# Optimization experiments

Measured on AMD Instinct MI355X. Metric: run time of the kernel, lower is better.

The kernel has to match this reference:

```python
import jax, jax.numpy as jnp
import numpy as np

D_MODEL = 2048
MLP = 8192
E = 8
R = 16
ALPHA = 32
SCALING = ALPHA / R  # lora_alpha / rank


def setup_inputs() -> dict:
    key = jax.random.key(0)
    ks = jax.random.split(key, 16)
    s = 0.02
    return {
        "x": jax.random.normal(ks[0], (4, 1024, D_MODEL), dtype=jnp.float32),
        # frozen base weights (nn.Linear stores [out, in])
        "w_gate": jax.random.normal(ks[1], (MLP, D_MODEL), dtype=jnp.float32) * s,
        "w_up": jax.random.normal(ks[2], (MLP, D_MODEL), dtype=jnp.float32) * s,
        "w_down": jax.random.normal(ks[3], (D_MODEL, MLP), dtype=jnp.float32) * s,
        # router
        "router_w": jax.random.normal(ks[4], (E, D_MODEL), dtype=jnp.float32) * s,
        "router_b": jnp.zeros((E,), dtype=jnp.float32),
        # LoRA expert params: A [E, r, fan_in], B [E, fan_out, r]
        "A_gate": jax.random.normal(ks[5], (E, R, D_MODEL), dtype=jnp.float32) * s,
        "B_gate": jax.random.normal(ks[6], (E, MLP, R), dtype=jnp.float32) * s,
        "A_up": jax.random.normal(ks[7], (E, R, D_MODEL), dtype=jnp.float32) * s,
        "B_up": jax.random.normal(ks[8], (E, MLP, R), dtype=jnp.float32) * s,
        "A_down": jax.random.normal(ks[9], (E, R, MLP), dtype=jnp.float32) * s,
        "B_down": jax.random.normal(ks[10], (E, D_MODEL, R), dtype=jnp.float32) * s,
    }


def _lora_moe_sparse(inp, W, A, B, onehot):
    # inp: [B,S,din], W: [dout,din], A: [E,r,din], B: [E,dout,r], onehot: [B,S,E]
    base = jnp.einsum("bsd,od->bso", inp, W)
    # low-rank projection for every expert is tiny: [B,S,E,r]
    t = jnp.einsum("bsd,erd->bser", inp, A)
    # top-1 dispatch: onehot zeroes out non-selected experts (== scatter assign,
    # since each token has exactly one expert)
    lora = jnp.einsum("bser,bse,eor->bso", t, onehot, B) * SCALING
    return base + lora


def reference(x, w_gate, w_up, w_down, router_w, router_b,
              A_gate, B_gate, A_up, B_up, A_down, B_down):
    logits = jnp.einsum("bsd,ed->bse", x, router_w) + router_b
    routing = jax.nn.softmax(logits, axis=-1)
    index = jnp.argmax(routing, axis=-1)                 # [B,S]
    y_hard = jax.nn.one_hot(index, E, dtype=logits.dtype)  # [B,S,E]
    expert_choice = y_hard - jax.lax.stop_gradient(routing) + routing

    gate_out = _lora_moe_sparse(x, w_gate, A_gate, B_gate, y_hard)
    up_out = _lora_moe_sparse(x, w_up, A_up, B_up, y_hard)
    h = jax.nn.silu(gate_out) * up_out
    out = _lora_moe_sparse(h, w_down, A_down, B_down, y_hard)
    return (out, routing, expert_choice)
```

## Files before the change

kernel.cpp:

```cpp
#include <hip/hip_runtime.h>
#include <stdint.h>

#define NTOK   4096
#define DM     2048
#define DMLP   8192
#define NEXP   8
#define NRANK  16
#define SCAL   2.0f

#define LDXA 2304
#define LDHA 8320

typedef __bf16 bf16x8 __attribute__((ext_vector_type(8)));
typedef float  f32x4  __attribute__((ext_vector_type(4)));
typedef unsigned short u16;

__device__ __forceinline__ u16 f2bf(float f) {
  unsigned u = __float_as_uint(f);
  u += 0x7fffu + ((u >> 16) & 1u);
  return (u16)(u >> 16);
}

__device__ __forceinline__ void gload_lds16(const void* g, void* l) {
  __builtin_amdgcn_global_load_lds((const __attribute__((address_space(1))) void*)g,
                                   (__attribute__((address_space(3))) void*)l, 16, 0, 0);
}

__global__ void cvt_kernel(const float* __restrict__ src, u16* __restrict__ dst, int n4) {
  int i = blockIdx.x * blockDim.x + threadIdx.x;
  int stride = gridDim.x * blockDim.x;
  for (; i < n4; i += stride) {
    float4 v = ((const float4*)src)[i];
    ushort4 o;
    o.x = f2bf(v.x); o.y = f2bf(v.y); o.z = f2bf(v.z); o.w = f2bf(v.w);
    ((ushort4*)dst)[i] = o;
  }
}

__global__ void build_wx(const float* __restrict__ W,
                         const float* __restrict__ Bm,
                         u16* __restrict__ dst,
                         int din, int ldx, int extoff, int browstride) {
  const int o = blockIdx.x;
  const int tid = threadIdx.x;
  u16* drow = dst + (size_t)o * ldx;
  const float* wrow = W + (size_t)o * din;
  for (int c4 = tid; c4 < din / 4; c4 += 256) {
    float4 v = ((const float4*)wrow)[c4];
    ushort4 ov;
    ov.x = f2bf(v.x); ov.y = f2bf(v.y); ov.z = f2bf(v.z); ov.w = f2bf(v.w);
    ((ushort4*)drow)[c4] = ov;
  }
  const int next = ldx - din;
  if (tid < next) {
    int c = tid;
    u16 val = 0;
    if (c >= extoff && c < extoff + NEXP * NRANK) {
      int ce = c - extoff;
      int e = ce >> 4, r = ce & 15;
      val = f2bf(Bm[((size_t)e * browstride + o) * NRANK + r]);
    }
    drow[din + c] = val;
  }
}

__global__ void router_kernel(const float* __restrict__ x,
                              const float* __restrict__ rw,
                              const float* __restrict__ rb,
                              u16* __restrict__ xa,
                              int* __restrict__ idx,
                              float* __restrict__ out_rout,
                              float* __restrict__ out_ec) {
  const int wave = threadIdx.x >> 6;
  const int lane = threadIdx.x & 63;
  const int m = blockIdx.x * 4 + wave;

  const float4* xrow = (const float4*)(x + (size_t)m * DM + lane * 32);
  float4 xv[8];
#pragma unroll
  for (int i = 0; i < 8; ++i) xv[i] = xrow[i];

  uint4 o[4];
  unsigned* op = (unsigned*)o;
#pragma unroll
  for (int i = 0; i < 8; ++i) {
    op[2*i]   = (unsigned)f2bf(xv[i].x) | ((unsigned)f2bf(xv[i].y) << 16);
    op[2*i+1] = (unsigned)f2bf(xv[i].z) | ((unsigned)f2bf(xv[i].w) << 16);
  }
  uint4* xdst = (uint4*)(xa + (size_t)m * LDXA + lane * 32);
#pragma unroll
  for (int i = 0; i < 4; ++i) xdst[i] = o[i];

  float lg[NEXP];
#pragma unroll
  for (int e = 0; e < NEXP; ++e) {
    const float4* wrow = (const float4*)(rw + (size_t)e * DM + lane * 32);
    float s = 0.f;
#pragma unroll
    for (int i = 0; i < 8; ++i) {
      float4 wv = wrow[i];
      s += xv[i].x*wv.x + xv[i].y*wv.y + xv[i].z*wv.z + xv[i].w*wv.w;
    }
#pragma unroll
    for (int off = 32; off > 0; off >>= 1) s += __shfl_xor(s, off, 64);
    lg[e] = s + rb[e];
  }

  float mx = lg[0];
#pragma unroll
  for (int e = 1; e < NEXP; ++e) mx = fmaxf(mx, lg[e]);
  float ex[NEXP], se = 0.f;
#pragma unroll
  for (int e = 0; e < NEXP; ++e) { ex[e] = expf(lg[e] - mx); se += ex[e]; }
  float inv = 1.f / se;
  int best = 0; float bv = lg[0];
#pragma unroll
  for (int e = 1; e < NEXP; ++e) if (lg[e] > bv) { bv = lg[e]; best = e; }

  if (lane == 0) {
    idx[m] = best;
#pragma unroll
    for (int e = 0; e < NEXP; ++e) {
      float r = ex[e] * inv;
      out_rout[(size_t)m * NEXP + e] = r;
      float hard = (e == best) ? 1.f : 0.f;
      out_ec[(size_t)m * NEXP + e] = (hard - r) + r;
    }
  }
}

template<int MODE>
__global__ __launch_bounds__(256, 2)
void gemm_kernel(const u16* __restrict__ A,
                 const u16* __restrict__ B0,
                 const int* __restrict__ idx,
                 void* __restrict__ Cout)
{
  constexpr int LDA = (MODE == 0) ? LDXA : LDHA;
  constexpr int LDB = (MODE == 0) ? 2048 : 8192;
  constexpr int NKI = (MODE == 0) ? 64 : 32;

  __shared__ u16 lds[16384];

  const int tid = threadIdx.x;
  const int w = tid >> 6;
  const int l = tid & 63;
  const int wm = w >> 1, wn = w & 1;
  const int mtile = blockIdx.x;
  const int ntile = (MODE == 3) ? 0 : (int)blockIdx.y;
  const int ks    = (MODE == 3) ? (int)blockIdx.y : 0;
  const int kb0   = (MODE == 3) ? ks * 1024 : 0;

  int srow[2];
  srow[0] = w * 16 + (l >> 2);
  srow[1] = 64 + srow[0];
  const int chunk = (l & 3) ^ ((srow[0] >> 1) & 3);
  const int scol = chunk * 8;

  const u16* aptr[2];
  const u16* bptr[2];
#pragma unroll
  for (int i = 0; i < 2; ++i) {
    aptr[i] = A + (size_t)(mtile * 128 + srow[i]) * LDA + kb0 + scol;
    bptr[i] = B0 + (size_t)(ntile * 128 + srow[i]) * LDB + kb0 + scol;
  }

  char* ldsc = (char*)lds;
  auto stage = [&](int buf, int kt) {
    const int kk = kt * 32;
    char* base = ldsc + buf * 16384;
#pragma unroll
    for (int i = 0; i < 2; ++i) {
      gload_lds16(aptr[i] + kk, base + i * 4096 + w * 1024);
      gload_lds16(bptr[i] + kk, base + 8192 + i * 4096 + w * 1024);
    }
  };

  f32x4 acc[4][4];
  f32x4 zf = {0.f, 0.f, 0.f, 0.f};
#pragma unroll
  for (int a = 0; a < 4; ++a)
#pragma unroll
    for (int b = 0; b < 4; ++b) acc[a][b] = zf;

  stage(0, 0);
  __syncthreads();

  const int kq   = l >> 4;
  const int arow = wm * 64 + (l & 15);
  const int brow = wn * 64 + (l & 15);
  const int axor = (kq ^ ((arow >> 1) & 3)) << 4;
  const int bxor = (kq ^ ((brow >> 1) & 3)) << 4;

  for (int kt = 0; kt < NKI; ++kt) {
    const int buf = kt & 1;
    if (kt + 1 < NKI) stage(buf ^ 1, kt + 1);
    const char* bA = ldsc + buf * 16384;
    const char* bB = bA + 8192;
    bf16x8 af[4], bfr[4];
#pragma unroll
    for (int fm = 0; fm < 4; ++fm)
      af[fm] = *(const bf16x8*)(bA + (arow + fm * 16) * 64 + axor);
#pragma unroll
    for (int fn = 0; fn < 4; ++fn)
      bfr[fn] = *(const bf16x8*)(bB + (brow + fn * 16) * 64 + bxor);
#pragma unroll
    for (int fm = 0; fm < 4; ++fm)
#pragma unroll
      for (int fn = 0; fn < 4; ++fn)
        acc[fm][fn] = __builtin_amdgcn_mfma_f32_16x16x32_bf16(af[fm], bfr[fn], acc[fm][fn], 0, 0, 0);
    __syncthreads();
  }

  const int lq = l >> 4;
  const int lr = l & 15;

  if (MODE == 0) {
    u16* X = (u16*)Cout;
#pragma unroll
    for (int fm = 0; fm < 4; ++fm)
#pragma unroll
      for (int fn = 0; fn < 4; ++fn)
        for (int j = 0; j < 4; ++j) {
          int m = mtile * 128 + wm * 64 + fm * 16 + lq * 4 + j;
          int c = ntile * 128 + wn * 64 + fn * 16 + lr;
          int e = idx[m];
          u16 v = (((c & 127) >> 4) == e) ? f2bf(SCAL * acc[fm][fn][j]) : (u16)0;
          X[(size_t)m * LDXA + 2048 + c] = v;
        }
  } else {
    float* P = (float*)Cout + (size_t)ks * NTOK * 128;
#pragma unroll
    for (int fm = 0; fm < 4; ++fm)
#pragma unroll
      for (int fn = 0; fn < 4; ++fn)
        for (int j = 0; j < 4; ++j) {
          int m = mtile * 128 + wm * 64 + fm * 16 + lq * 4 + j;
          int c = wn * 64 + fn * 16 + lr;
          P[(size_t)m * 128 + c] = acc[fm][fn][j];
        }
  }
}

__global__ __launch_bounds__(512, 2)
void gemm_gu(const u16* __restrict__ Ag,
             const u16* __restrict__ B0g,
             const u16* __restrict__ B1g,
             u16* __restrict__ H)
{
  constexpr int NKT = 36;
  __shared__ char L[131072];

  const int tid = threadIdx.x, w = tid >> 6, l = tid & 63;
  const int wm = w >> 2, wn = w & 3;
  const int bid = blockIdx.x;
  const int rr = bid >> 3;
  const int mtile = rr >> 3;
  const int ntile = (bid & 7) * 8 + (rr & 7);

  const u16 *agb0, *agb1, *bgb0, *bgb1;
  {
    int row0 = tid >> 2, row1 = 128 + row0;
    int lc = (tid & 3) ^ ((row0 >> 1) & 3);
    agb0 = Ag + (size_t)(mtile * 256 + row0) * LDXA + lc * 8;
    agb1 = Ag + (size_t)(mtile * 256 + row1) * LDXA + lc * 8;
    int c0 = ntile * 128 + ((row0 >> 5) << 4) + (row0 & 15);
    int c1 = ntile * 128 + ((row1 >> 5) << 4) + (row1 & 15);
    bgb0 = (((row0 >> 4) & 1) ? B1g : B0g) + (size_t)c0 * LDXA + lc * 8;
    bgb1 = (((row1 >> 4) & 1) ? B1g : B0g) + (size_t)c1 * LDXA + lc * 8;
  }
  const int sdst = w * 1024;

#define STGA(z, kt) { const int ko_ = ((kt) < NKT ? (kt) : NKT - 1) * 64 + ((z) & 1) * 32; \
    gload_lds16(agb0 + ko_, L + (z) * 16384 + sdst); \
    gload_lds16(agb1 + ko_, L + (z) * 16384 + 8192 + sdst); }
#define STGB(z, kt) { const int ko_ = ((kt) < NKT ? (kt) : NKT - 1) * 64 + ((z) & 1) * 32; \
    gload_lds16(bgb0 + ko_, L + 65536 + (z) * 16384 + sdst); \
    gload_lds16(bgb1 + ko_, L + 65536 + (z) * 16384 + 8192 + sdst); }

  const int lr = l & 15;
  const int kob = (((l >> 4) ^ ((lr >> 1) & 3)) << 4);
  const int abase = (wm * 128 + lr) * 64 + kob;
  const int bbase = (wn * 64 + lr) * 64 + kob;

  bf16x8 A0_[4], A1_[4], B0_[4], B1_[4];
#define RDA(S, z, qa) _Pragma("unroll") for (int f = 0; f < 4; ++f) \
    S[f] = *(const bf16x8*)(L + (z) * 16384 + abase + (qa) * 4096 + f * 1024);
#define RDB(S, z) _Pragma("unroll") for (int f = 0; f < 4; ++f) \
    S[f] = *(const bf16x8*)(L + 65536 + (z) * 16384 + bbase + f * 1024);

  f32x4 acc[8][4];
  f32x4 zf = {0.f, 0.f, 0.f, 0.f};
#pragma unroll
  for (int a = 0; a < 8; ++a)
#pragma unroll
    for (int b = 0; b < 4; ++b) acc[a][b] = zf;

#define MF(qa, AS, BS) \
  __builtin_amdgcn_s_setprio(1); \
  _Pragma("unroll") for (int f = 0; f < 4; ++f) \
    _Pragma("unroll") for (int n = 0; n < 4; ++n) \
      acc[(qa) * 4 + f][n] = __builtin_amdgcn_mfma_f32_16x16x32_bf16(AS[f], BS[n], acc[(qa) * 4 + f][n], 0, 0, 0); \
  __builtin_amdgcn_s_setprio(0);

#define VMW  { asm volatile("s_waitcnt vmcnt(6)" ::: "memory"); __builtin_amdgcn_sched_barrier(0); }
#define PEND { __builtin_amdgcn_sched_barrier(0); __builtin_amdgcn_s_barrier(); __builtin_amdgcn_sched_barrier(0); }

  STGA(0, 0) STGB(0, 0)
  STGA(1, 0) STGB(1, 0)
  STGA(2, 1) STGB(2, 1)
  VMW
  PEND
  RDB(B0_, 0) RDA(A0_, 0, 0)

  for (int it = 0; it < NKT / 2; ++it) {
    const int k1 = 2 * it + 1, k2 = 2 * it + 2, k3 = 2 * it + 3;
    STGA(3, k1)  VMW
    RDA(A1_, 0, 1)
    MF(0, A0_, B0_)  PEND
    STGB(3, k1)
    RDB(B1_, 1) RDA(A0_, 1, 0)
    MF(1, A1_, B0_)  PEND
    STGA(0, k2)  VMW
    RDA(A1_, 1, 1)
    MF(0, A0_, B1_)  PEND
    STGB(0, k2)
    RDB(B0_, 2) RDA(A0_, 2, 0)
    MF(1, A1_, B1_)  PEND
    STGA(1, k2)  VMW
    RDA(A1_, 2, 1)
    MF(0, A0_, B0_)  PEND
    STGB(1, k2)
    RDB(B1_, 3) RDA(A0_, 3, 0)
    MF(1, A1_, B0_)  PEND
    STGA(2, k3)  VMW
    RDA(A1_, 3, 1)
    MF(0, A0_, B1_)  PEND
    STGB(2, k3)
    RDB(B0_, 0) RDA(A0_, 0, 0)
    MF(1, A1_, B1_)  PEND
  }

  const int lq = l >> 4;
#pragma unroll
  for (int fm = 0; fm < 8; ++fm)
    for (int jj = 0; jj < 4; ++jj) {
      const int m = mtile * 256 + wm * 128 + fm * 16 + lq * 4 + jj;
#pragma unroll
      for (int p = 0; p < 2; ++p) {
        float g = acc[fm][2 * p][jj];
        float u = acc[fm][2 * p + 1][jj];
        float e = __builtin_amdgcn_exp2f(g * -1.44269504089f);
        float h = g * __builtin_amdgcn_rcpf(1.f + e) * u;
        const int c = ntile * 128 + (wn * 2 + p) * 16 + lr;
        H[(size_t)m * LDHA + c] = f2bf(h);
      }
    }
#undef RDA
#undef RDB
#undef MF
#undef STGA
#undef STGB
#undef VMW
#undef PEND
}

__global__ __launch_bounds__(512, 2)
void gemm6(const u16* __restrict__ Ag,
           const u16* __restrict__ Bg,
           float* __restrict__ C)
{
  __shared__ char L[147456];
  const int tid = threadIdx.x, w = tid >> 6, l = tid & 63;
  const int wm = w >> 2, wn = w & 3;
  const int bid = blockIdx.x;
  const int swz = (bid & 7) * 32 + (bid >> 3);
  const int mtile = swz >> 3;
  const int ntile = swz & 7;

  const u16 *agb0, *bgb0, *bgb1;
  {
    int row0 = tid >> 2;
    int lc = (tid & 3) ^ ((row0 >> 1) & 3);
    agb0 = Ag + (size_t)(mtile * 128 + row0) * LDHA + lc * 8;
    bgb0 = Bg + (size_t)(ntile * 256 + row0) * LDHA + lc * 8;
    bgb1 = Bg + (size_t)(ntile * 256 + 128 + row0) * LDHA + lc * 8;
  }
  const int sdst = w * 1024;

#define STG6(z, g) { const int gg_ = (g) < 260 ? (g) : 259; \
    const int ko_ = (gg_ >> 1) * 64 + (gg_ & 1) * 32; \
    gload_lds16(agb0 + ko_, L + (z) * 24576 + sdst); \
    gload_lds16(bgb0 + ko_, L + (z) * 24576 + 8192 + sdst); \
    gload_lds16(bgb1 + ko_, L + (z) * 24576 + 16384 + sdst); }

  const int lr = l & 15;
  const int kob = (((l >> 4) ^ ((lr >> 1) & 3)) << 4);
  const int abase = (wm * 64 + lr) * 64 + kob;
  const int bbase = (wn * 64 + lr) * 64 + kob;

  bf16x8 A0_[4], A1_[4], B0_[4], B1_[4];
#define RDA6(S, z) _Pragma("unroll") for (int f = 0; f < 4; ++f) \
    S[f] = *(const bf16x8*)(L + (z) * 24576 + abase + f * 1024);
#define RDB6(S, z) _Pragma("unroll") for (int f = 0; f < 4; ++f) \
    S[f] = *(const bf16x8*)(L + (z) * 24576 + 8192 + bbase + f * 1024);

  f32x4 acc[4][4];
  f32x4 zf = {0.f, 0.f, 0.f, 0.f};
#pragma unroll
  for (int a = 0; a < 4; ++a)
#pragma unroll
    for (int b = 0; b < 4; ++b) acc[a][b] = zf;

#define MF6(AS, BS) \
  __builtin_amdgcn_s_setprio(1); \
  _Pragma("unroll") for (int f = 0; f < 4; ++f) \
    _Pragma("unroll") for (int n = 0; n < 4; ++n) \
      acc[f][n] = __builtin_amdgcn_mfma_f32_16x16x32_bf16(AS[f], BS[n], acc[f][n], 0, 0, 0); \
  __builtin_amdgcn_s_setprio(0);

#define VMW6 { asm volatile("s_waitcnt vmcnt(6)" ::: "memory"); __builtin_amdgcn_sched_barrier(0); }
#define PEND6 { __builtin_amdgcn_sched_barrier(0); __builtin_amdgcn_s_barrier(); __builtin_amdgcn_sched_barrier(0); }

  STG6(0, 0) STG6(1, 1) STG6(2, 2) STG6(3, 3)
  VMW6
  PEND6
  RDB6(B0_, 0) RDA6(A0_, 0)

  for (int it = 0; it < 43; ++it) {
    const int g4 = it * 6 + 4;
    STG6(4, g4)      VMW6  RDB6(B1_, 1) RDA6(A1_, 1)  MF6(A0_, B0_)  PEND6
    STG6(5, g4 + 1)  VMW6  RDB6(B0_, 2) RDA6(A0_, 2)  MF6(A1_, B1_)  PEND6
    STG6(0, g4 + 2)  VMW6  RDB6(B1_, 3) RDA6(A1_, 3)  MF6(A0_, B0_)  PEND6
    STG6(1, g4 + 3)  VMW6  RDB6(B0_, 4) RDA6(A0_, 4)  MF6(A1_, B1_)  PEND6
    STG6(2, g4 + 4)  VMW6  RDB6(B1_, 5) RDA6(A1_, 5)  MF6(A0_, B0_)  PEND6
    STG6(3, g4 + 5)  VMW6  RDB6(B0_, 0) RDA6(A0_, 0)  MF6(A1_, B1_)  PEND6
  }
  RDB6(B1_, 1) RDA6(A1_, 1)
  MF6(A0_, B0_)
  MF6(A1_, B1_)

  const int lq = l >> 4;
#pragma unroll
  for (int fm = 0; fm < 4; ++fm)
#pragma unroll
    for (int n = 0; n < 4; ++n)
      for (int jj = 0; jj < 4; ++jj) {
        const int m = mtile * 128 + wm * 64 + fm * 16 + lq * 4 + jj;
        const int c = ntile * 256 + wn * 64 + n * 16 + lr;
        C[(size_t)m * DM + c] = acc[fm][n][jj];
      }
#undef RDA6
#undef RDB6
#undef MF6
#undef STG6
#undef VMW6
#undef PEND6
}

__global__ void td_reduce(const float* __restrict__ part,
                          const int* __restrict__ idx,
                          u16* __restrict__ ha) {
  int i = blockIdx.x * blockDim.x + threadIdx.x;
  int m = i >> 7, c = i & 127;
  float s = 0.f;
#pragma unroll
  for (int k = 0; k < 8; ++k) s += part[(size_t)k * NTOK * 128 + i];
  u16 v = ((c >> 4) == idx[m]) ? f2bf(SCAL * s) : (u16)0;
  ha[(size_t)m * LDHA + 8192 + c] = v;
}

extern "C" void kernel_launch(void* const* d_in, const int* in_sizes, int n_in,
                              void* d_out, int out_size, void* d_ws, size_t ws_size,
                              hipStream_t stream) {
  const float* x  = (const float*)d_in[0];
  const float* wg = (const float*)d_in[1];
  const float* wu = (const float*)d_in[2];
  const float* wd = (const float*)d_in[3];
  const float* rw = (const float*)d_in[4];
  const float* rb = (const float*)d_in[5];
  const float* Ag = (const float*)d_in[6];
  const float* Bg = (const float*)d_in[7];
  const float* Au = (const float*)d_in[8];
  const float* Bu = (const float*)d_in[9];
  const float* Ad = (const float*)d_in[10];
  const float* Bd = (const float*)d_in[11];

  float* out      = (float*)d_out;
  float* out_rout = out + (size_t)NTOK * DM;
  float* out_ec   = out_rout + (size_t)NTOK * NEXP;

  char* ws = (char*)d_ws;
  size_t off = 0;
  auto take = [&](size_t b) { void* p = ws + off; off += (b + 255) & ~(size_t)255; return p; };
  u16*   xa   = (u16*)take((size_t)NTOK * LDXA * 2);
  u16*   ha   = (u16*)take((size_t)NTOK * LDHA * 2);
  u16*   wgx  = (u16*)take((size_t)DMLP * LDXA * 2);
  u16*   wux  = (u16*)take((size_t)DMLP * LDXA * 2);
  u16*   wdx  = (u16*)take((size_t)DM * LDHA * 2);
  u16*   Aab  = (u16*)take((size_t)256 * DM * 2);
  u16*   Adb  = (u16*)take((size_t)128 * DMLP * 2);
  float* tdp  = (float*)take((size_t)8 * NTOK * 128 * 4);
  int*   idx  = (int*)take((size_t)NTOK * 4);
  if (off > ws_size) return;

  cvt_kernel<<<64, 256, 0, stream>>>(Ag, Aab, 128 * DM / 4);
  cvt_kernel<<<64, 256, 0, stream>>>(Au, Aab + 128 * DM, 128 * DM / 4);
  cvt_kernel<<<128, 256, 0, stream>>>(Ad, Adb, 128 * DMLP / 4);

  build_wx<<<DMLP, 256, 0, stream>>>(wg, Bg, wgx, DM, LDXA, 0,   DMLP);
  build_wx<<<DMLP, 256, 0, stream>>>(wu, Bu, wux, DM, LDXA, 128, DMLP);
  build_wx<<<DM,   256, 0, stream>>>(wd, Bd, wdx, DMLP, LDHA, 0, DM);

  router_kernel<<<NTOK / 4, 256, 0, stream>>>(x, rw, rb, xa, idx, out_rout, out_ec);

  gemm_kernel<0><<<dim3(32, 2), 256, 0, stream>>>(xa, Aab, idx, xa);
  gemm_gu<<<1024, 512, 0, stream>>>(xa, wgx, wux, ha);
  gemm_kernel<3><<<dim3(32, 8), 256, 0, stream>>>(ha, Adb, idx, tdp);
  td_reduce<<<NTOK * 128 / 256, 256, 0, stream>>>(tdp, idx, ha);
  gemm6<<<256, 512, 0, stream>>>(ha, wdx, out);
}
```

Measured before the change: 579.9 us.

## Fuse weight prep kernels and defer vmcnt waits past MFMA blocks

Replaces six separate conversion and weight-packing launches with a single grid-stride prep kernel that converts the base weights, LoRA A matrices and LoRA B extension columns to bf16. In the gate/up and down GEMM main loops, the s_waitcnt on outstanding global-to-LDS loads is moved from before the LDS reads and MFMA issue to just before the barrier, so memory latency can overlap with the matrix math. Both aim to cut launch overhead and pipeline stalls. The risk is that the fused prep kernel's strided access pattern is less efficient, and that the later wait changes the correctness assumptions of the LDS ring buffer.

```diff
diff --git a/kernel.cpp b/kernel.cpp
--- a/kernel.cpp
+++ b/kernel.cpp
@@ -26,41 +26,56 @@
                                    (__attribute__((address_space(3))) void*)l, 16, 0, 0);
 }
 
-__global__ void cvt_kernel(const float* __restrict__ src, u16* __restrict__ dst, int n4) {
-  int i = blockIdx.x * blockDim.x + threadIdx.x;
-  int stride = gridDim.x * blockDim.x;
-  for (; i < n4; i += stride) {
-    float4 v = ((const float4*)src)[i];
-    ushort4 o;
-    o.x = f2bf(v.x); o.y = f2bf(v.y); o.z = f2bf(v.z); o.w = f2bf(v.w);
-    ((ushort4*)dst)[i] = o;
-  }
-}
-
-__global__ void build_wx(const float* __restrict__ W,
-                         const float* __restrict__ Bm,
-                         u16* __restrict__ dst,
-                         int din, int ldx, int extoff, int browstride) {
-  const int o = blockIdx.x;
-  const int tid = threadIdx.x;
-  u16* drow = dst + (size_t)o * ldx;
-  const float* wrow = W + (size_t)o * din;
-  for (int c4 = tid; c4 < din / 4; c4 += 256) {
-    float4 v = ((const float4*)wrow)[c4];
-    ushort4 ov;
+__global__ void prep_kernel(const float* __restrict__ wg, const float* __restrict__ wu,
+                            const float* __restrict__ wd,
+                            const float* __restrict__ Ag, const float* __restrict__ Au,
+                            const float* __restrict__ Ad,
+                            const float* __restrict__ Bg, const float* __restrict__ Bu,
+                            const float* __restrict__ Bd,
+                            u16* __restrict__ wgx, u16* __restrict__ wux,
+                            u16* __restrict__ wdx, u16* __restrict__ Aab,
+                            u16* __restrict__ Adb) {
+  const int gt = blockIdx.x * blockDim.x + threadIdx.x;
+  const int gs = gridDim.x * blockDim.x;
+
+  for (int i = gt; i < DMLP * 512; i += gs) {
+    const int o = i >> 9, c = (i & 511) << 2;
+    float4 v = ((const float4*)wg)[i];
+    ushort4 ov; ov.x = f2bf(v.x); ov.y = f2bf(v.y); ov.z = f2bf(v.z); ov.w = f2bf(v.w);
+    *(ushort4*)(wgx + (size_t)o * LDXA + c) = ov;
+    v = ((const float4*)wu)[i];
     ov.x = f2bf(v.x); ov.y = f2bf(v.y); ov.z = f2bf(v.z); ov.w = f2bf(v.w);
-    ((ushort4*)drow)[c4] = ov;
-  }
-  const int next = ldx - din;
-  if (tid < next) {
-    int c = tid;
-    u16 val = 0;
-    if (c >= extoff && c < extoff + NEXP * NRANK) {
-      int ce = c - extoff;
-      int e = ce >> 4, r = ce & 15;
-      val = f2bf(Bm[((size_t)e * browstride + o) * NRANK + r]);
-    }
-    drow[din + c] = val;
+    *(ushort4*)(wux + (size_t)o * LDXA + c) = ov;
+  }
+  for (int i = gt; i < DM * 2048; i += gs) {
+    const int o = i >> 11, c = (i & 2047) << 2;
+    float4 v = ((const float4*)wd)[i];
+    ushort4 ov; ov.x = f2bf(v.x); ov.y = f2bf(v.y); ov.z = f2bf(v.z); ov.w = f2bf(v.w);
+    *(ushort4*)(wdx + (size_t)o * LDHA + c) = ov;
+  }
+  for (int i = gt; i < 256 * 512; i += gs) {
+    float4 v = (i < 128 * 512) ? ((const float4*)Ag)[i] : ((const float4*)Au)[i - 128 * 512];
+    ushort4 ov; ov.x = f2bf(v.x); ov.y = f2bf(v.y); ov.z = f2bf(v.z); ov.w = f2bf(v.w);
+    ((ushort4*)Aab)[i] = ov;
+  }
+  for (int i = gt; i < 128 * 2048; i += gs) {
+    float4 v = ((const float4*)Ad)[i];
+    ushort4 ov; ov.x = f2bf(v.x); ov.y = f2bf(v.y); ov.z = f2bf(v.z); ov.w = f2bf(v.w);
+    ((ushort4*)Adb)[i] = ov;
+  }
+  for (int i = gt; i < DMLP * 256; i += gs) {
+    const int o = i >> 8, c = i & 255;
+    const int e = (c & 127) >> 4, r = c & 15;
+    u16 vg = 0, vu = 0;
+    if (c < 128) vg = f2bf(Bg[((size_t)e * DMLP + o) * NRANK + r]);
+    else         vu = f2bf(Bu[((size_t)e * DMLP + o) * NRANK + r]);
+    wgx[(size_t)o * LDXA + 2048 + c] = vg;
+    wux[(size_t)o * LDXA + 2048 + c] = vu;
+  }
+  for (int i = gt; i < DM * 128; i += gs) {
+    const int o = i >> 7, c = i & 127;
+    const int e = c >> 4, r = c & 15;
+    wdx[(size_t)o * LDHA + 8192 + c] = f2bf(Bd[((size_t)e * DM + o) * NRANK + r]);
   }
 }
 
@@ -315,27 +330,27 @@
 
   for (int it = 0; it < NKT / 2; ++it) {
     const int k1 = 2 * it + 1, k2 = 2 * it + 2, k3 = 2 * it + 3;
-    STGA(3, k1)  VMW
+    STGA(3, k1)
     RDA(A1_, 0, 1)
-    MF(0, A0_, B0_)  PEND
+    MF(0, A0_, B0_)  VMW  PEND
     STGB(3, k1)
     RDB(B1_, 1) RDA(A0_, 1, 0)
     MF(1, A1_, B0_)  PEND
-    STGA(0, k2)  VMW
+    STGA(0, k2)
     RDA(A1_, 1, 1)
-    MF(0, A0_, B1_)  PEND
+    MF(0, A0_, B1_)  VMW  PEND
     STGB(0, k2)
     RDB(B0_, 2) RDA(A0_, 2, 0)
     MF(1, A1_, B1_)  PEND
-    STGA(1, k2)  VMW
+    STGA(1, k2)
     RDA(A1_, 2, 1)
-    MF(0, A0_, B0_)  PEND
+    MF(0, A0_, B0_)  VMW  PEND
     STGB(1, k2)
     RDB(B1_, 3) RDA(A0_, 3, 0)
     MF(1, A1_, B0_)  PEND
-    STGA(2, k3)  VMW
+    STGA(2, k3)
     RDA(A1_, 3, 1)
-    MF(0, A0_, B1_)  PEND
+    MF(0, A0_, B1_)  VMW  PEND
     STGB(2, k3)
     RDB(B0_, 0) RDA(A0_, 0, 0)
     MF(1, A1_, B1_)  PEND
@@ -429,12 +444,12 @@
 
   for (int it = 0; it < 43; ++it) {
     const int g4 = it * 6 + 4;
-    STG6(4, g4)      VMW6  RDB6(B1_, 1) RDA6(A1_, 1)  MF6(A0_, B0_)  PEND6
-    STG6(5, g4 + 1)  VMW6  RDB6(B0_, 2) RDA6(A0_, 2)  MF6(A1_, B1_)  PEND6
-    STG6(0, g4 + 2)  VMW6  RDB6(B1_, 3) RDA6(A1_, 3)  MF6(A0_, B0_)  PEND6
-    STG6(1, g4 + 3)  VMW6  RDB6(B0_, 4) RDA6(A0_, 4)  MF6(A1_, B1_)  PEND6
-    STG6(2, g4 + 4)  VMW6  RDB6(B1_, 5) RDA6(A1_, 5)  MF6(A0_, B0_)  PEND6
-    STG6(3, g4 + 5)  VMW6  RDB6(B0_, 0) RDA6(A0_, 0)  MF6(A1_, B1_)  PEND6
+    STG6(4, g4)      RDB6(B1_, 1) RDA6(A1_, 1)  MF6(A0_, B0_)  VMW6  PEND6
+    STG6(5, g4 + 1)  RDB6(B0_, 2) RDA6(A0_, 2)  MF6(A1_, B1_)  VMW6  PEND6
+    STG6(0, g4 + 2)  RDB6(B1_, 3) RDA6(A1_, 3)  MF6(A0_, B0_)  VMW6  PEND6
+    STG6(1, g4 + 3)  RDB6(B0_, 4) RDA6(A0_, 4)  MF6(A1_, B1_)  VMW6  PEND6
+    STG6(2, g4 + 4)  RDB6(B1_, 5) RDA6(A1_, 5)  MF6(A0_, B0_)  VMW6  PEND6
+    STG6(3, g4 + 5)  RDB6(B0_, 0) RDA6(A0_, 0)  MF6(A1_, B1_)  VMW6  PEND6
   }
   RDB6(B1_, 1) RDA6(A1_, 1)
   MF6(A0_, B0_)
@@ -504,13 +519,8 @@
   int*   idx  = (int*)take((size_t)NTOK * 4);
   if (off > ws_size) return;
 
-  cvt_kernel<<<64, 256, 0, stream>>>(Ag, Aab, 128 * DM / 4);
-  cvt_kernel<<<64, 256, 0, stream>>>(Au, Aab + 128 * DM, 128 * DM / 4);
-  cvt_kernel<<<128, 256, 0, stream>>>(Ad, Adb, 128 * DMLP / 4);
-
-  build_wx<<<DMLP, 256, 0, stream>>>(wg, Bg, wgx, DM, LDXA, 0,   DMLP);
-  build_wx<<<DMLP, 256, 0, stream>>>(wu, Bu, wux, DM, LDXA, 128, DMLP);
-  build_wx<<<DM,   256, 0, stream>>>(wd, Bd, wdx, DMLP, LDHA, 0, DM);
+  prep_kernel<<<2048, 256, 0, stream>>>(wg, wu, wd, Ag, Au, Ad, Bg, Bu, Bd,
+                                        wgx, wux, wdx, Aab, Adb);
 
   router_kernel<<<NTOK / 4, 256, 0, stream>>>(x, rw, rb, xa, idx, out_rout, out_ec);
 
```

After: 556.7 us. 1.04x faster.
